# Performance work log

Hardware: AMD Instinct MI355X
Metric: run time of the kernel (lower is better)

Reference implementation:

```python
import jax, jax.numpy as jnp
import numpy as np

B, T, D, H = 2, 2048, 1024, 16
HD = D // H
SCALE = HD ** -0.5
NEG_INF = float(np.finfo(np.float32).min)


def setup_inputs() -> dict:
    key = jax.random.key(0)
    ks = jax.random.split(key, 10)
    s = 1.0 / np.sqrt(D)
    x = jax.random.normal(ks[0], (B, T, D), dtype=jnp.float32)
    # causal mask, True = keep, shape (B,1,T,T)
    mask = jnp.broadcast_to(jnp.tril(jnp.ones((T, T), dtype=bool)), (B, 1, T, T))
    Wq = jax.random.normal(ks[1], (D, D), dtype=jnp.float32) * s
    bq = jax.random.normal(ks[2], (D,), dtype=jnp.float32) * s
    Wk = jax.random.normal(ks[3], (D, D), dtype=jnp.float32) * s
    bk = jax.random.normal(ks[4], (D,), dtype=jnp.float32) * s
    Wv = jax.random.normal(ks[5], (D, D), dtype=jnp.float32) * s
    bv = jax.random.normal(ks[6], (D,), dtype=jnp.float32) * s
    Wo = jax.random.normal(ks[7], (D, D), dtype=jnp.float32) * s
    bo = jax.random.normal(ks[8], (D,), dtype=jnp.float32) * s
    return {"x": x, "mask": mask, "Wq": Wq, "bq": bq, "Wk": Wk, "bk": bk,
            "Wv": Wv, "bv": bv, "Wo": Wo, "bo": bo}


def _split_heads(t):
    # (B,T,D) -> (B,H,T,HD)
    return t.reshape(B, T, H, HD).transpose(0, 2, 1, 3)


def masked_rowwise_softmax(scores, mask):
    # mask: bool, True = keep; fully-masked rows return zeros.
    s = scores.astype(jnp.float32)
    masked = jnp.where(mask, s, NEG_INF)
    row_max = jnp.max(masked, axis=-1, keepdims=True)
    exps = jnp.exp(masked - row_max) * mask.astype(jnp.float32)
    denom = jnp.maximum(jnp.sum(exps, axis=-1, keepdims=True), 1e-12)
    return (exps / denom).astype(scores.dtype)


def reference(x, mask, Wq, bq, Wk, bk, Wv, bv, Wo, bo):
    q = _split_heads(x @ Wq.T + bq)
    k = _split_heads(x @ Wk.T + bk)
    v = _split_heads(x @ Wv.T + bv)
    scores = jnp.einsum('bhqd,bhkd->bhqk', q, k) * SCALE
    m = jnp.broadcast_to(mask, (B, H, T, T))
    attn = masked_rowwise_softmax(scores, m)
    y = jnp.einsum('bhqk,bhkd->bhqd', attn, v)
    y = y.transpose(0, 2, 1, 3).reshape(B, T, D)
    return y @ Wo.T + bo
```

## Files before the change

### kernel.cpp

```cpp
#include <hip/hip_runtime.h>

#define B_ 2
#define H_ 16
#define T_ 2048
#define D_ 1024
#define HD_ 64
#define NEG_HUGE (-3.402823466e38f)
#define QSCALE 0.18033688011112042f

typedef unsigned short u16;
typedef unsigned int u32;
typedef __attribute__((ext_vector_type(8))) short bf16x8;
typedef __attribute__((ext_vector_type(4))) float f32x4;

__device__ __forceinline__ u16 f2bf(float f) {
    u32 u = __builtin_bit_cast(u32, f);
    u += 0x7FFFu + ((u >> 16) & 1u);
    return (u16)(u >> 16);
}

__device__ __forceinline__ u32 pk2bf(float f0, float f1) {
    const u32 a0 = __builtin_bit_cast(u32, f0) + 0x8000u;
    const u32 a1 = __builtin_bit_cast(u32, f1) + 0x8000u;
    return __builtin_amdgcn_perm(a1, a0, 0x07060302u);
}

__device__ __forceinline__ uint2 pk4bf(f32x4 a) {
    uint2 r;
    r.x = pk2bf(a[0], a[1]);
    r.y = pk2bf(a[2], a[3]);
    return r;
}

__device__ __forceinline__ f32x4 mfma16(bf16x8 a, bf16x8 b, f32x4 c) {
    return __builtin_amdgcn_mfma_f32_16x16x32_bf16(a, b, c, 0, 0, 0);
}

__global__ __launch_bounds__(256) void to_bf16(
    const float* __restrict__ x,  const float* __restrict__ wq,
    const float* __restrict__ wk, const float* __restrict__ wv,
    const float* __restrict__ wo, u16* __restrict__ dst)
{
    const size_t g = ((size_t)blockIdx.x * 256 + threadIdx.x) * 8;
    const float* src; size_t off;
    if      (g < (size_t)(4u << 20)) { src = x;  off = g; }
    else if (g < (size_t)(5u << 20)) { src = wq; off = g - (size_t)(4u << 20); }
    else if (g < (size_t)(6u << 20)) { src = wk; off = g - (size_t)(5u << 20); }
    else if (g < (size_t)(7u << 20)) { src = wv; off = g - (size_t)(6u << 20); }
    else                             { src = wo; off = g - (size_t)(7u << 20); }
    const float4 a = *(const float4*)&src[off];
    const float4 b = *(const float4*)&src[off + 4];
    ushort4 lo = make_ushort4(f2bf(a.x), f2bf(a.y), f2bf(a.z), f2bf(a.w));
    ushort4 hi = make_ushort4(f2bf(b.x), f2bf(b.y), f2bf(b.z), f2bf(b.w));
    *(ushort4*)&dst[g]     = lo;
    *(ushort4*)&dst[g + 4] = hi;
}

__device__ __forceinline__ void gemm128_core(
    const u16* __restrict__ P0, const u16* __restrict__ P1,
    const int m0, const int n0, u16* As, u16* Bs, f32x4 (&acc)[4][4])
{
    const int tid  = threadIdx.x;
    const int lane = tid & 63;
    const int quad = lane >> 4;
    const int l15  = lane & 15;
    const int w    = tid >> 6;
    const int wm   = (w >> 1) << 6;
    const int wn   = (w & 1) << 6;
    const int swz  = l15 & 7;

    size_t aoff[4], boff[4];
    int    loff[4];
#pragma unroll
    for (int i = 0; i < 4; ++i) {
        const int slot = i * 256 + tid;
        const int r = slot >> 3, c = slot & 7;
        const int gc = (c ^ (r & 7)) << 3;
        aoff[i] = (size_t)(m0 + r) * D_ + gc;
        boff[i] = (size_t)(n0 + r) * D_ + gc;
        loff[i] = slot * 8;
    }
    int rowA[4], rowB[4];
#pragma unroll
    for (int i = 0; i < 4; ++i) {
        rowA[i] = (wm + i * 16 + l15) * 64;
        rowB[i] = (wn + i * 16 + l15) * 64;
    }

    bf16x8 pa[4], pb[4];
#pragma unroll
    for (int i = 0; i < 4; ++i) {
        pa[i] = *(const bf16x8*)&P0[aoff[i]];
        pb[i] = *(const bf16x8*)&P1[boff[i]];
    }

    for (int k0 = 0; k0 < D_; k0 += 64) {
        __syncthreads();
#pragma unroll
        for (int i = 0; i < 4; ++i) {
            *(bf16x8*)&As[loff[i]] = pa[i];
            *(bf16x8*)&Bs[loff[i]] = pb[i];
        }
        if (k0 + 64 < D_) {
            const int kn = k0 + 64;
#pragma unroll
            for (int i = 0; i < 4; ++i) {
                pa[i] = *(const bf16x8*)&P0[aoff[i] + kn];
                pb[i] = *(const bf16x8*)&P1[boff[i] + kn];
            }
        }
        __syncthreads();
#pragma unroll
        for (int s = 0; s < 2; ++s) {
            const int ch = (((s << 2) + quad) ^ swz) << 3;
            bf16x8 am[4], bm[4];
#pragma unroll
            for (int mi = 0; mi < 4; ++mi) am[mi] = *(const bf16x8*)&As[rowA[mi] + ch];
#pragma unroll
            for (int ni = 0; ni < 4; ++ni) bm[ni] = *(const bf16x8*)&Bs[rowB[ni] + ch];
#pragma unroll
            for (int mi = 0; mi < 4; ++mi)
#pragma unroll
                for (int ni = 0; ni < 4; ++ni)
                    acc[mi][ni] = mfma16(am[mi], bm[ni], acc[mi][ni]);
        }
    }
}

__global__ __launch_bounds__(256) void gemm_qkv(
    const u16* __restrict__ xb,
    const u16* __restrict__ Wqb, const u16* __restrict__ Wkb, const u16* __restrict__ Wvb,
    const float* __restrict__ bq, const float* __restrict__ bk, const float* __restrict__ bv,
    u16* __restrict__ Qb, u16* __restrict__ Kb, u16* __restrict__ Vtb)
{
    __shared__ u16 As[128 * 64];
    __shared__ u16 Bs[128 * 64];
    const int L   = blockIdx.x;
    const int xcd = L & 7;
    const int kk  = L >> 3;
    const int tt  = (xcd << 2) + (kk & 3);
    const int ft  = (kk >> 2) & 7;
    const int z   = kk >> 5;

    f32x4 acc[4][4];
#pragma unroll
    for (int i = 0; i < 4; ++i)
#pragma unroll
        for (int j = 0; j < 4; ++j) acc[i][j] = (f32x4){0.f, 0.f, 0.f, 0.f};

    const int tid  = threadIdx.x;
    const int lane = tid & 63;
    const int quad = lane >> 4;
    const int l15  = lane & 15;
    const int w    = tid >> 6;
    const int wm   = (w >> 1) << 6;
    const int wn   = (w & 1) << 6;
    const int pq   = quad >> 1;
    const int psub = (quad & 1) << 2;

    u16* scr = ((w < 2) ? As : Bs) + ((w & 1) ? 4096 : 0);

    if (z < 2) {
        const u16*   W    = z ? Wkb : Wqb;
        const float* bias = z ? bk  : bq;
        const float  CF   = z ? 1.f : QSCALE;
        u16*         C    = z ? Kb  : Qb;
        const int m0 = ft << 7;
        const int n0 = tt << 7;
        gemm128_core(W, xb, m0, n0, As, Bs, acc);
        __syncthreads();

        const int fb = m0 + wm;
        const int h  = fb >> 6;
        const int tb = n0 + wn;
#pragma unroll
        for (int i = 0; i < 4; ++i) {
            const float4 bi = *(const float4*)&bias[fb + i * 16 + (quad << 2)];
#pragma unroll
            for (int j = 0; j < 4; ++j) {
                const int tl = j * 16 + l15;
                f32x4 a = acc[i][j];
                f32x4 v = { (a[0] + bi.x) * CF, (a[1] + bi.y) * CF,
                            (a[2] + bi.z) * CF, (a[3] + bi.w) * CF };
                *(uint2*)&scr[tl * 64 + (((2 * i + pq) ^ (tl & 7)) << 3) + psub] = pk4bf(v);
            }
        }
        __asm__ volatile("s_waitcnt lgkmcnt(0)" ::: "memory");

        const int b  = tb >> 11;
        const int t0 = tb & 2047;
#pragma unroll
        for (int e = 0; e < 8; ++e) {
            const int tl = (lane >> 3) + e * 8;
            const int c  = lane & 7;
            bf16x8 v = *(const bf16x8*)&scr[tl * 64 + ((c ^ (tl & 7)) << 3)];
            *(bf16x8*)&C[((size_t)((b << 4) + h) * T_ + t0 + tl) * HD_ + (c << 3)] = v;
        }
    } else {
        const int m0 = tt << 7;
        const int n0 = ft << 7;
        gemm128_core(xb, Wvb, m0, n0, As, Bs, acc);
        __syncthreads();

#pragma unroll
        for (int j = 0; j < 4; ++j) {
            const int row = j * 16 + l15;
            const float bi = bv[n0 + wn + row];
            const int sw = row & 7;
#pragma unroll
            for (int i = 0; i < 4; ++i) {
                f32x4 a = acc[i][j];
                f32x4 v = { a[0] + bi, a[1] + bi, a[2] + bi, a[3] + bi };
                *(uint2*)&scr[row * 64 + (((2 * i + pq) ^ sw) << 3) + psub] = pk4bf(v);
            }
        }
        __asm__ volatile("s_waitcnt lgkmcnt(0)" ::: "memory");

        const int b  = (m0 + wm) >> 11;
        const int t0 = (m0 + wm) & 2047;
        const int h  = (n0 + wn) >> 6;
#pragma unroll
        for (int e = 0; e < 8; ++e) {
            const int hdl = (lane >> 3) + e * 8;
            const int c   = lane & 7;
            bf16x8 vv = *(const bf16x8*)&scr[hdl * 64 + ((c ^ (hdl & 7)) << 3)];
            *(bf16x8*)&Vtb[((size_t)((b << 4) + h) * HD_ + hdl) * T_ + t0 + (c << 3)] = vv;
        }
    }
}

__global__ __launch_bounds__(256) void gemm_out(
    const u16* __restrict__ Ab, const u16* __restrict__ Wob,
    const float* __restrict__ bo, float* __restrict__ C)
{
    __shared__ u16 As[128 * 64];
    __shared__ u16 Bs[128 * 64];
    const int L   = blockIdx.x;
    const int xcd = L & 7;
    const int kk  = L >> 3;
    const int tt  = (xcd << 2) + (kk & 3);
    const int ft  = kk >> 2;
    const int m0  = tt << 7;
    const int n0  = ft << 7;

    f32x4 acc[4][4];
#pragma unroll
    for (int i = 0; i < 4; ++i)
#pragma unroll
        for (int j = 0; j < 4; ++j) acc[i][j] = (f32x4){0.f, 0.f, 0.f, 0.f};

    gemm128_core(Ab, Wob, m0, n0, As, Bs, acc);

    const int tid  = threadIdx.x;
    const int lane = tid & 63;
    const int quad = lane >> 4;
    const int l15  = lane & 15;
    const int w    = tid >> 6;
    const int wm   = (w >> 1) << 6;
    const int wn   = (w & 1) << 6;

    float bi[4];
#pragma unroll
    for (int ni = 0; ni < 4; ++ni) bi[ni] = bo[n0 + wn + ni * 16 + l15];

#pragma unroll
    for (int mi = 0; mi < 4; ++mi) {
        const int m = m0 + wm + mi * 16 + (quad << 2);
#pragma unroll
        for (int r = 0; r < 4; ++r)
#pragma unroll
            for (int ni = 0; ni < 4; ++ni)
                C[(size_t)(m + r) * D_ + n0 + wn + ni * 16 + l15] = acc[mi][ni][r] + bi[ni];
    }
}

__global__ __launch_bounds__(256) void attn_mfma(
    const u16* __restrict__ Qg, const u16* __restrict__ Kg,
    const u16* __restrict__ Vtg, u16* __restrict__ Out)
{
    __shared__ u16 Ks[128 * 64];
    __shared__ u16 Vs[64 * 128];
    __shared__ u16 Ps[4 * 16 * 128];
    const int tid  = threadIdx.x;
    const int w    = tid >> 6;
    const int lane = tid & 63;
    const int quad = lane >> 4;
    const int l15  = lane & 15;
    const int bh   = blockIdx.x;
    const int yb   = blockIdx.y;
    const size_t base = (size_t)bh * (T_ * HD_);

    int lK[4], lV[4];
    size_t gK[4], gV[4];
#pragma unroll
    for (int i = 0; i < 4; ++i) {
        const int slot = i * 256 + tid;
        const int rk = slot >> 3, ck = slot & 7;
        lK[i] = rk * 64 + ((ck ^ (rk & 7)) << 3);
        gK[i] = base + (size_t)rk * HD_ + ck * 8;
        const int rv = slot >> 4, cv = slot & 15;
        lV[i] = rv * 128 + ((cv ^ (rv & 15)) << 3);
        gV[i] = base + (size_t)rv * T_ + cv * 8;
    }

    bf16x8 ones;
#pragma unroll
    for (int i = 0; i < 8; ++i) ones[i] = (short)0x3F80;

    u16* Pw = &Ps[w * 2048];
    const int swz7 = l15 & 7;
    const int pq   = quad >> 1;
    const int psub = (quad & 1) << 2;
    const int b = bh >> 4, h = bh & 15;

    for (int half = 0; half < 2; ++half) {
        const int qt = half ? yb : (31 - yb);
        const int qloc = (w << 4) + l15;
        const int qrow = (qt << 6) + qloc;
        const bf16x8 qf0 = *(const bf16x8*)&Qg[base + (size_t)qrow * HD_ + quad * 8];
        const bf16x8 qf1 = *(const bf16x8*)&Qg[base + (size_t)qrow * HD_ + 32 + quad * 8];

        f32x4 o[4];
#pragma unroll
        for (int nt = 0; nt < 4; ++nt) o[nt] = (f32x4){0.f, 0.f, 0.f, 0.f};
        f32x4 Lacc = (f32x4){0.f, 0.f, 0.f, 0.f};

        const int nIter = (qt + 2) >> 1;
        bf16x8 kreg[4], vreg[4];
#pragma unroll
        for (int i = 0; i < 4; ++i) {
            kreg[i] = *(const bf16x8*)&Kg[gK[i]];
            vreg[i] = *(const bf16x8*)&Vtg[gV[i]];
        }

        for (int it = 0; it < nIter; ++it) {
            __syncthreads();
#pragma unroll
            for (int i = 0; i < 4; ++i) {
                *(bf16x8*)&Ks[lK[i]] = kreg[i];
                *(bf16x8*)&Vs[lV[i]] = vreg[i];
            }
            if (it + 1 < nIter) {
                const int koff = (it + 1) << 7;
#pragma unroll
                for (int i = 0; i < 4; ++i) {
                    kreg[i] = *(const bf16x8*)&Kg[gK[i] + (size_t)koff * HD_];
                    vreg[i] = *(const bf16x8*)&Vtg[gV[i] + koff];
                }
            }
            __syncthreads();

            f32x4 st[8];
#pragma unroll
            for (int t = 0; t < 8; ++t) {
                const int kr = (t * 16 + l15) * 64;
                const bf16x8 k0 = *(const bf16x8*)&Ks[kr + ((quad ^ swz7) << 3)];
                const bf16x8 k1 = *(const bf16x8*)&Ks[kr + (((quad + 4) ^ swz7) << 3)];
                f32x4 a = (f32x4){0.f, 0.f, 0.f, 0.f};
                a = mfma16(k0, qf0, a);
                a = mfma16(k1, qf1, a);
                st[t] = a;
            }

            if (it == nIter - 1) {
                const int koff = it << 7;
#pragma unroll
                for (int t = 0; t < 8; ++t)
#pragma unroll
                    for (int r = 0; r < 4; ++r) {
                        const int kg = koff + t * 16 + (quad << 2) + r;
                        if (kg > qrow) st[t][r] = NEG_HUGE;
                    }
            }

#pragma unroll
            for (int t = 0; t < 8; ++t)
#pragma unroll
                for (int r = 0; r < 4; ++r) st[t][r] = exp2f(st[t][r]);

#pragma unroll
            for (int t = 0; t < 8; ++t)
                *(uint2*)&Pw[l15 * 128 + (((2 * t + pq) ^ l15) << 3) + psub] = pk4bf(st[t]);
            __asm__ volatile("s_waitcnt lgkmcnt(0)" ::: "memory");

            bf16x8 pf[4];
#pragma unroll
            for (int kq = 0; kq < 4; ++kq)
                pf[kq] = *(const bf16x8*)&Pw[l15 * 128 + ((((kq << 2) + quad) ^ l15) << 3)];

#pragma unroll
            for (int nt = 0; nt < 4; ++nt) {
                f32x4 oo = o[nt];
                const int vr = (nt * 16 + l15) * 128;
#pragma unroll
                for (int kq = 0; kq < 4; ++kq) {
                    const bf16x8 vf = *(const bf16x8*)&Vs[vr + ((((kq << 2) + quad) ^ l15) << 3)];
                    oo = mfma16(pf[kq], vf, oo);
                }
                o[nt] = oo;
            }
#pragma unroll
            for (int kq = 0; kq < 4; ++kq)
                Lacc = mfma16(pf[kq], ones, Lacc);
        }

        f32x4 linv;
#pragma unroll
        for (int r = 0; r < 4; ++r) linv[r] = 1.f / fmaxf(Lacc[r], 1e-30f);

#pragma unroll
        for (int nt = 0; nt < 4; ++nt)
#pragma unroll
            for (int r = 0; r < 4; ++r) {
                const int qg2 = (qt << 6) + (w << 4) + (quad << 2) + r;
                const u32 u = __builtin_bit_cast(u32, o[nt][r] * linv[r]) + 0x8000u;
                Out[(size_t)(b * T_ + qg2) * D_ + (h << 6) + nt * 16 + l15] = (u16)(u >> 16);
            }
    }
}

extern "C" void kernel_launch(void* const* d_in, const int* in_sizes, int n_in,
                              void* d_out, int out_size, void* d_ws, size_t ws_size,
                              hipStream_t stream)
{
    const float* x  = (const float*)d_in[0];
    const float* Wq = (const float*)d_in[2];
    const float* bq = (const float*)d_in[3];
    const float* Wk = (const float*)d_in[4];
    const float* bk = (const float*)d_in[5];
    const float* Wv = (const float*)d_in[6];
    const float* bv = (const float*)d_in[7];
    const float* Wo = (const float*)d_in[8];
    const float* bo = (const float*)d_in[9];
    float* out = (float*)d_out;

    const size_t M1 = (size_t)1 << 20;
    u16* wsu = (u16*)d_ws;
    u16* xb  = wsu;
    u16* wqb = wsu + 4 * M1;
    u16* wkb = wsu + 5 * M1;
    u16* wvb = wsu + 6 * M1;
    u16* wob = wsu + 7 * M1;
    u16* Qb  = wsu + 8 * M1;
    u16* Kb  = wsu + 12 * M1;
    u16* Vtb = wsu + 16 * M1;
    u16* AOb = wsu + 20 * M1;

    to_bf16<<<4096, 256, 0, stream>>>(x, Wq, Wk, Wv, Wo, wsu);

    gemm_qkv<<<768, 256, 0, stream>>>(xb, wqb, wkb, wvb, bq, bk, bv, Qb, Kb, Vtb);

    dim3 ga(B_ * H_, T_ / 128);
    attn_mfma<<<ga, 256, 0, stream>>>(Qb, Kb, Vtb, AOb);

    gemm_out<<<256, 256, 0, stream>>>(AOb, wob, bo, out);
}
```

Measured before the change: 195.5 us.

## Make attention waves independent, streaming K/V from global without shared staging

The attention kernel drops the block-shared K/V tiles in LDS and the two __syncthreads per iteration. Each wave now owns one 16-row query tile and loads its own K and V fragments straight from global memory into registers, 64 keys per step. Work is mapped longest-first over a flat 1024-block grid, and diagonal tiles skip the fully masked MFMAs. This removes barriers and LDS traffic, but K/V reuse across the four waves now depends on cache hits, so global and L2 load traffic goes up and global latency is exposed inside each wave.

New measurement: 278.0 us. 1.42x slower.

```diff
diff --git a/kernel.cpp b/kernel.cpp
--- a/kernel.cpp
+++ b/kernel.cpp
@@ -278,145 +278,143 @@
     const u16* __restrict__ Qg, const u16* __restrict__ Kg,
     const u16* __restrict__ Vtg, u16* __restrict__ Out)
 {
-    __shared__ u16 Ks[128 * 64];
-    __shared__ u16 Vs[64 * 128];
-    __shared__ u16 Ps[4 * 16 * 128];
+    __shared__ u16 Ps[4 * 16 * 64];
     const int tid  = threadIdx.x;
     const int w    = tid >> 6;
     const int lane = tid & 63;
     const int quad = lane >> 4;
     const int l15  = lane & 15;
-    const int bh   = blockIdx.x;
-    const int yb   = blockIdx.y;
+    const int id   = blockIdx.x;
+    const int bh   = id & 31;
+    const int lb   = id >> 5;
+    const int j    = 127 - ((lb << 2) + w);
     const size_t base = (size_t)bh * (T_ * HD_);
 
-    int lK[4], lV[4];
-    size_t gK[4], gV[4];
-#pragma unroll
-    for (int i = 0; i < 4; ++i) {
-        const int slot = i * 256 + tid;
-        const int rk = slot >> 3, ck = slot & 7;
-        lK[i] = rk * 64 + ((ck ^ (rk & 7)) << 3);
-        gK[i] = base + (size_t)rk * HD_ + ck * 8;
-        const int rv = slot >> 4, cv = slot & 15;
-        lV[i] = rv * 128 + ((cv ^ (rv & 15)) << 3);
-        gV[i] = base + (size_t)rv * T_ + cv * 8;
-    }
+    const int qrow = (j << 4) + l15;
+    const bf16x8 qf0 = *(const bf16x8*)&Qg[base + (size_t)qrow * HD_ + quad * 8];
+    const bf16x8 qf1 = *(const bf16x8*)&Qg[base + (size_t)qrow * HD_ + 32 + quad * 8];
+
+    f32x4 o[4];
+#pragma unroll
+    for (int nt = 0; nt < 4; ++nt) o[nt] = (f32x4){0.f, 0.f, 0.f, 0.f};
+    f32x4 Lacc = (f32x4){0.f, 0.f, 0.f, 0.f};
+
+    const int nIter = (j >> 2) + 1;
+    const int jm    = j & 3;
 
     bf16x8 ones;
 #pragma unroll
     for (int i = 0; i < 8; ++i) ones[i] = (short)0x3F80;
 
-    u16* Pw = &Ps[w * 2048];
-    const int swz7 = l15 & 7;
+    u16* Pw = &Ps[w * 1024];
+    const int swz  = l15 & 7;
     const int pq   = quad >> 1;
     const int psub = (quad & 1) << 2;
-    const int b = bh >> 4, h = bh & 15;
-
-    for (int half = 0; half < 2; ++half) {
-        const int qt = half ? yb : (31 - yb);
-        const int qloc = (w << 4) + l15;
-        const int qrow = (qt << 6) + qloc;
-        const bf16x8 qf0 = *(const bf16x8*)&Qg[base + (size_t)qrow * HD_ + quad * 8];
-        const bf16x8 qf1 = *(const bf16x8*)&Qg[base + (size_t)qrow * HD_ + 32 + quad * 8];
-
-        f32x4 o[4];
-#pragma unroll
-        for (int nt = 0; nt < 4; ++nt) o[nt] = (f32x4){0.f, 0.f, 0.f, 0.f};
-        f32x4 Lacc = (f32x4){0.f, 0.f, 0.f, 0.f};
-
-        const int nIter = (qt + 2) >> 1;
-        bf16x8 kreg[4], vreg[4];
-#pragma unroll
-        for (int i = 0; i < 4; ++i) {
-            kreg[i] = *(const bf16x8*)&Kg[gK[i]];
-            vreg[i] = *(const bf16x8*)&Vtg[gV[i]];
-        }
-
-        for (int it = 0; it < nIter; ++it) {
-            __syncthreads();
-#pragma unroll
-            for (int i = 0; i < 4; ++i) {
-                *(bf16x8*)&Ks[lK[i]] = kreg[i];
-                *(bf16x8*)&Vs[lV[i]] = vreg[i];
-            }
-            if (it + 1 < nIter) {
-                const int koff = (it + 1) << 7;
-#pragma unroll
-                for (int i = 0; i < 4; ++i) {
-                    kreg[i] = *(const bf16x8*)&Kg[gK[i] + (size_t)koff * HD_];
-                    vreg[i] = *(const bf16x8*)&Vtg[gV[i] + koff];
-                }
-            }
-            __syncthreads();
-
-            f32x4 st[8];
-#pragma unroll
-            for (int t = 0; t < 8; ++t) {
-                const int kr = (t * 16 + l15) * 64;
-                const bf16x8 k0 = *(const bf16x8*)&Ks[kr + ((quad ^ swz7) << 3)];
-                const bf16x8 k1 = *(const bf16x8*)&Ks[kr + (((quad + 4) ^ swz7) << 3)];
+
+    size_t kadr[4][2], vadr[4][2];
+#pragma unroll
+    for (int t = 0; t < 4; ++t)
+#pragma unroll
+        for (int c = 0; c < 2; ++c) {
+            kadr[t][c] = base + (size_t)(t * 16 + l15) * HD_ + c * 32 + quad * 8;
+            vadr[t][c] = base + (size_t)(t * 16 + l15) * T_  + c * 32 + quad * 8;
+        }
+
+    bf16x8 kf[4][2];
+#pragma unroll
+    for (int t = 0; t < 4; ++t)
+#pragma unroll
+        for (int c = 0; c < 2; ++c)
+            kf[t][c] = *(const bf16x8*)&Kg[kadr[t][c]];
+
+    bool mcond[4];
+#pragma unroll
+    for (int r = 0; r < 4; ++r) mcond[r] = ((quad << 2) + r) > l15;
+
+    for (int it = 0; it < nIter; ++it) {
+        const bool last = (it == nIter - 1);
+        const int  tmax = last ? jm : 3;
+
+        f32x4 st[4];
+#pragma unroll
+        for (int t = 0; t < 4; ++t) {
+            if (t <= tmax) {
                 f32x4 a = (f32x4){0.f, 0.f, 0.f, 0.f};
-                a = mfma16(k0, qf0, a);
-                a = mfma16(k1, qf1, a);
+                a = mfma16(kf[t][0], qf0, a);
+                a = mfma16(kf[t][1], qf1, a);
                 st[t] = a;
             }
-
-            if (it == nIter - 1) {
-                const int koff = it << 7;
-#pragma unroll
-                for (int t = 0; t < 8; ++t)
-#pragma unroll
-                    for (int r = 0; r < 4; ++r) {
-                        const int kg = koff + t * 16 + (quad << 2) + r;
-                        if (kg > qrow) st[t][r] = NEG_HUGE;
-                    }
+        }
+
+        if (!last) {
+            const size_t koff = (size_t)(it + 1) * 64 * HD_;
+#pragma unroll
+            for (int t = 0; t < 4; ++t)
+#pragma unroll
+                for (int c = 0; c < 2; ++c)
+                    kf[t][c] = *(const bf16x8*)&Kg[kadr[t][c] + koff];
+        }
+
+        uint2 px[4];
+#pragma unroll
+        for (int t = 0; t < 4; ++t) {
+            if (t <= tmax) {
+                if (last && t == jm) {
+#pragma unroll
+                    for (int r = 0; r < 4; ++r)
+                        if (mcond[r]) st[t][r] = NEG_HUGE;
+                }
+#pragma unroll
+                for (int r = 0; r < 4; ++r) st[t][r] = exp2f(st[t][r]);
+                px[t] = pk4bf(st[t]);
+            } else {
+                px[t] = make_uint2(0u, 0u);
             }
-
-#pragma unroll
-            for (int t = 0; t < 8; ++t)
-#pragma unroll
-                for (int r = 0; r < 4; ++r) st[t][r] = exp2f(st[t][r]);
-
-#pragma unroll
-            for (int t = 0; t < 8; ++t)
-                *(uint2*)&Pw[l15 * 128 + (((2 * t + pq) ^ l15) << 3) + psub] = pk4bf(st[t]);
-            __asm__ volatile("s_waitcnt lgkmcnt(0)" ::: "memory");
-
-            bf16x8 pf[4];
-#pragma unroll
-            for (int kq = 0; kq < 4; ++kq)
-                pf[kq] = *(const bf16x8*)&Pw[l15 * 128 + ((((kq << 2) + quad) ^ l15) << 3)];
-
-#pragma unroll
-            for (int nt = 0; nt < 4; ++nt) {
-                f32x4 oo = o[nt];
-                const int vr = (nt * 16 + l15) * 128;
-#pragma unroll
-                for (int kq = 0; kq < 4; ++kq) {
-                    const bf16x8 vf = *(const bf16x8*)&Vs[vr + ((((kq << 2) + quad) ^ l15) << 3)];
-                    oo = mfma16(pf[kq], vf, oo);
-                }
-                o[nt] = oo;
-            }
-#pragma unroll
-            for (int kq = 0; kq < 4; ++kq)
-                Lacc = mfma16(pf[kq], ones, Lacc);
-        }
-
-        f32x4 linv;
-#pragma unroll
-        for (int r = 0; r < 4; ++r) linv[r] = 1.f / fmaxf(Lacc[r], 1e-30f);
-
+        }
+
+#pragma unroll
+        for (int t = 0; t < 4; ++t)
+            *(uint2*)&Pw[l15 * 64 + ((((t << 1) + pq) ^ swz) << 3) + psub] = px[t];
+
+        bf16x8 vf[4][2];
+        const size_t voff = (size_t)it * 64;
 #pragma unroll
         for (int nt = 0; nt < 4; ++nt)
 #pragma unroll
-            for (int r = 0; r < 4; ++r) {
-                const int qg2 = (qt << 6) + (w << 4) + (quad << 2) + r;
-                const u32 u = __builtin_bit_cast(u32, o[nt][r] * linv[r]) + 0x8000u;
-                Out[(size_t)(b * T_ + qg2) * D_ + (h << 6) + nt * 16 + l15] = (u16)(u >> 16);
-            }
-    }
+            for (int c = 0; c < 2; ++c)
+                vf[nt][c] = *(const bf16x8*)&Vtg[vadr[nt][c] + voff];
+
+        __asm__ volatile("s_waitcnt lgkmcnt(0)" ::: "memory");
+
+        bf16x8 pf[2];
+#pragma unroll
+        for (int c = 0; c < 2; ++c)
+            pf[c] = *(const bf16x8*)&Pw[l15 * 64 + ((((c << 2) + quad) ^ swz) << 3)];
+
+#pragma unroll
+        for (int nt = 0; nt < 4; ++nt) {
+            f32x4 oo = o[nt];
+            oo = mfma16(pf[0], vf[nt][0], oo);
+            oo = mfma16(pf[1], vf[nt][1], oo);
+            o[nt] = oo;
+        }
+        Lacc = mfma16(pf[0], ones, Lacc);
+        Lacc = mfma16(pf[1], ones, Lacc);
+    }
+
+    f32x4 linv;
+#pragma unroll
+    for (int r = 0; r < 4; ++r) linv[r] = 1.f / fmaxf(Lacc[r], 1e-30f);
+
+    const int b = bh >> 4, h = bh & 15;
+#pragma unroll
+    for (int nt = 0; nt < 4; ++nt)
+#pragma unroll
+        for (int r = 0; r < 4; ++r) {
+            const int qg2 = (j << 4) + (quad << 2) + r;
+            const u32 u = __builtin_bit_cast(u32, o[nt][r] * linv[r]) + 0x8000u;
+            Out[(size_t)(b * T_ + qg2) * D_ + (h << 6) + nt * 16 + l15] = (u16)(u >> 16);
+        }
 }
 
 extern "C" void kernel_launch(void* const* d_in, const int* in_sizes, int n_in,
@@ -450,8 +448,7 @@
 
     gemm_qkv<<<768, 256, 0, stream>>>(xb, wqb, wkb, wvb, bq, bk, bv, Qb, Kb, Vtb);
 
-    dim3 ga(B_ * H_, T_ / 128);
-    attn_mfma<<<ga, 256, 0, stream>>>(Qb, Kb, Vtb, AOb);
+    attn_mfma<<<1024, 256, 0, stream>>>(Qb, Kb, Vtb, AOb);
 
     gemm_out<<<256, 256, 0, stream>>>(AOb, wob, bo, out);
 }
```
